# Performance work log

Measured on AMD Instinct MI355X. Metric: run time of the kernel, lower is better.

## Reference

```python
import jax, jax.numpy as jnp
from jax import lax
import numpy as np


def _rnn_tanh_layer(x, W_ih, W_hh, b_ih, b_hh, return_seq):
    # x: [B, T, I]; W_ih: [H, I]; W_hh: [H, H]
    B = x.shape[0]
    H = W_hh.shape[0]
    # Precompute input projection for all timesteps (one big GEMM).
    xw = jnp.einsum('bti,hi->bth', x, W_ih) + b_ih + b_hh  # [B, T, H]
    xw_t = jnp.swapaxes(xw, 0, 1)  # [T, B, H] for scan
    h0 = jnp.zeros((B, H), dtype=x.dtype)

    def step(h, xt):
        h_new = jnp.tanh(xt + h @ W_hh.T)
        return h_new, (h_new if return_seq else None)

    hT, hs = lax.scan(step, h0, xw_t)
    if return_seq:
        return jnp.swapaxes(hs, 0, 1), hT  # [B, T, H], [B, H]
    return None, hT


def setup_inputs() -> dict:
    key = jax.random.key(0)
    ks = jax.random.split(key, 12)
    B, T, I, H1, H2, C = 512, 1024, 32, 128, 64, 10

    def unif(k, shape, fan):
        bound = 1.0 / np.sqrt(fan)
        return jax.random.uniform(k, shape, jnp.float32, -bound, bound)

    return {
        'x': jax.random.normal(ks[0], (B, T, I), jnp.float32),
        'W_ih1': unif(ks[1], (H1, I), H1),
        'W_hh1': unif(ks[2], (H1, H1), H1),
        'b_ih1': unif(ks[3], (H1,), H1),
        'b_hh1': unif(ks[4], (H1,), H1),
        'W_ih2': unif(ks[5], (H2, H1), H2),
        'W_hh2': unif(ks[6], (H2, H2), H2),
        'b_ih2': unif(ks[7], (H2,), H2),
        'b_hh2': unif(ks[8], (H2,), H2),
        'W_fc': unif(ks[9], (C, H2), H2),
        'b_fc': unif(ks[10], (C,), H2),
    }


def reference(x, W_ih1, W_hh1, b_ih1, b_hh1, W_ih2, W_hh2, b_ih2, b_hh2, W_fc, b_fc):
    out1, _h1 = _rnn_tanh_layer(x, W_ih1, W_hh1, b_ih1, b_hh1, return_seq=True)
    _none, h2 = _rnn_tanh_layer(out1, W_ih2, W_hh2, b_ih2, b_hh2, return_seq=False)
    # Dropout(p=0.3) is identity in eval mode.
    logits = h2 @ W_fc.T + b_fc  # [B, 10]
    return logits
```

## Files before the change

kernel.cpp:

```cpp
#include <hip/hip_runtime.h>
#include <stdint.h>


typedef _Float16 f16x8 __attribute__((ext_vector_type(8)));
typedef _Float16 f16x4 __attribute__((ext_vector_type(4)));
typedef float f32x4 __attribute__((ext_vector_type(4)));

#define MFMA_F16(A, B, C) __builtin_amdgcn_mfma_f32_16x16x32_f16((A), (B), (C), 0, 0, 0)

__device__ __forceinline__ float tanh_fast(float x) {
  float t = __builtin_amdgcn_exp2f(x * 2.88539008177792681472f);
  return 1.0f - 2.0f * __builtin_amdgcn_rcpf(t + 1.0f);
}

__device__ __forceinline__ uint32_t pk16(float a, float b) {
  return __builtin_bit_cast(uint32_t, __builtin_amdgcn_cvt_pkrtz(a, b));
}

__device__ __forceinline__ void sync_lds() {
  asm volatile("s_waitcnt lgkmcnt(0)\n\ts_barrier" ::: "memory");
}

__device__ __forceinline__ f16x8 cvt8w(const float* s) {
  f32x4 a = *(const f32x4*)s;
  f32x4 b = *(const f32x4*)(s + 4);
  f16x8 r;
#pragma unroll
  for (int j = 0; j < 4; ++j) { r[j] = (_Float16)a[j]; r[4 + j] = (_Float16)b[j]; }
  return r;
}

__device__ __forceinline__ f16x8 pack_x8(const f32x4& a, const f32x4& b) {
  union { uint32_t u[4]; f16x8 v; } tmp;
  tmp.u[0] = pk16(a[0], a[1]); tmp.u[1] = pk16(a[2], a[3]);
  tmp.u[2] = pk16(b[0], b[1]); tmp.u[3] = pk16(b[2], b[3]);
  return tmp.v;
}

__global__ __launch_bounds__(256) void xw_pre(
    const float* __restrict__ x, const float* __restrict__ Wih1,
    const float* __restrict__ bih1, const float* __restrict__ bhh1,
    uint2* __restrict__ xw)
{
  const int tid  = threadIdx.x;
  const int w    = tid >> 6, lane = tid & 63;
  const int g    = lane >> 4, n = lane & 15;
  const int gb   = blockIdx.x >> 3;
  const int t0   = ((blockIdx.x & 7) << 7) + (w << 5);

  f16x8 aI[8];
  f32x4 bias[8];
#pragma unroll
  for (int m = 0; m < 8; ++m) {
    aI[m] = cvt8w(Wih1 + (m * 16 + n) * 32 + g * 8);
#pragma unroll
    for (int r = 0; r < 4; ++r)
      bias[m][r] = bih1[m * 16 + g * 4 + r] + bhh1[m * 16 + g * 4 + r];
  }

  const float* xp = x + ((size_t)(gb * 16 + n) * 1024 + t0) * 32 + g * 8;
  uint2* xo = xw + (size_t)(gb * 1024 + t0) * 512 + lane;

  f32x4 xa = *(const f32x4*)(xp);
  f32x4 xb = *(const f32x4*)(xp + 4);
  for (int tt = 0; tt < 32; ++tt) {
    f32x4 na, nb;
    if (tt < 31) {
      na = *(const f32x4*)(xp + (tt + 1) * 32);
      nb = *(const f32x4*)(xp + (tt + 1) * 32 + 4);
    }
    f16x8 xf = pack_x8(xa, xb);
#pragma unroll
    for (int m = 0; m < 8; ++m) {
      f32x4 d = MFMA_F16(aI[m], xf, bias[m]);
      xo[tt * 512 + m * 64] = make_uint2(pk16(d[0], d[1]), pk16(d[2], d[3]));
    }
    xa = na; xb = nb;
  }
}

template <bool USE_XW>
__global__ __attribute__((amdgpu_waves_per_eu(2, 2))) __launch_bounds__(512)
void rnn_rec(
    const float* __restrict__ x,
    const float* __restrict__ Wih1, const float* __restrict__ Whh1,
    const float* __restrict__ bih1, const float* __restrict__ bhh1,
    const float* __restrict__ Wih2, const float* __restrict__ Whh2,
    const float* __restrict__ bih2, const float* __restrict__ bhh2,
    const float* __restrict__ Wfc,  const float* __restrict__ bfc,
    const uint2* __restrict__ xw,
    float* __restrict__ out)
{
  constexpr int T = 1024, I = 32, H1 = 128, H2 = 64, BB = 16;
  constexpr int R1 = 272, R2 = 144;
  constexpr int H1_0 = 0, H1_1 = 4352;
  constexpr int H2_0 = 8704, H2_1 = 11008;
  constexpr int H2F  = 13312;
  __shared__ __align__(16) unsigned char smem[17408];

  const int tid  = threadIdx.x;
  const int w    = tid >> 6;
  const int lane = tid & 63;
  const int g    = lane >> 4;
  const int n    = lane & 15;
  const int b0   = blockIdx.x * BB;

  {
    uint32_t* p = (uint32_t*)smem;
    for (int i = tid; i < 1088; i += 512) p[i] = 0u;
    uint32_t* q = (uint32_t*)(smem + H2_0);
    for (int i = tid; i < 576; i += 512) q[i] = 0u;
  }

  int roff1[4];
#pragma unroll
  for (int k4 = 0; k4 < 4; ++k4)
    roff1[k4] = n * R1 + k4 * 64 + g * 16;

  auto tanh_pack = [&](const f32x4& a, uint32_t& lo, uint32_t& hi) {
    lo = pk16(tanh_fast(a[0]), tanh_fast(a[1]));
    hi = pk16(tanh_fast(a[2]), tanh_fast(a[3]));
  };

  __syncthreads();

  const f32x4 zero = {0.f, 0.f, 0.f, 0.f};

  if (w < 4) {
    f16x8 aU[2][4];
#pragma unroll
    for (int ti = 0; ti < 2; ++ti) {
      const int ch = (2 * w + ti) * 16 + n;
#pragma unroll
      for (int k4 = 0; k4 < 4; ++k4)
        aU[ti][k4] = cvt8w(Whh1 + ch * H1 + k4 * 32 + g * 8);
    }
    int woff[2];
#pragma unroll
    for (int ti = 0; ti < 2; ++ti)
      woff[ti] = n * R1 + (2 * w + ti) * 32 + g * 8;

    if constexpr (USE_XW) {
      const uint2* xwp = xw + (size_t)blockIdx.x * T * 512 + lane;
      const int ti0 = (2 * w) * 64, ti1 = (2 * w + 1) * 64;

      auto cvtC = [](uint2 v) -> f32x4 {
        f16x4 h = __builtin_bit_cast(f16x4, v);
        f32x4 r;
#pragma unroll
        for (int i = 0; i < 4; ++i) r[i] = (float)h[i];
        return r;
      };

      uint2 qA0 = xwp[0 * 512 + ti0], qA1 = xwp[0 * 512 + ti1];
      uint2 qB0 = xwp[1 * 512 + ti0], qB1 = xwp[1 * 512 + ti1];

      auto stepL1 = [&](int t, int cur, uint2& s0, uint2& s1) {
        const char* H1c = (const char*)smem + (cur ? H1_1 : H1_0);
        char*       H1n = (char*)smem + (cur ? H1_0 : H1_1);
        f16x8 b1k0 = *(const f16x8*)(H1c + roff1[0]);
        f16x8 b1k1 = *(const f16x8*)(H1c + roff1[1]);
        f16x8 b1k2 = *(const f16x8*)(H1c + roff1[2]);
        f16x8 b1k3 = *(const f16x8*)(H1c + roff1[3]);
        f32x4 accI0 = cvtC(s0), accI1 = cvtC(s1);
        if (t + 2 < T) {
          s0 = xwp[(t + 2) * 512 + ti0];
          s1 = xwp[(t + 2) * 512 + ti1];
        }
        f32x4 aA0 = MFMA_F16(aU[0][0], b1k0, accI0);
        f32x4 aB0 = MFMA_F16(aU[0][2], b1k2, zero);
        f32x4 aA1 = MFMA_F16(aU[1][0], b1k0, accI1);
        f32x4 aB1 = MFMA_F16(aU[1][2], b1k2, zero);
        aA0 = MFMA_F16(aU[0][1], b1k1, aA0);
        aB0 = MFMA_F16(aU[0][3], b1k3, aB0);
        aA1 = MFMA_F16(aU[1][1], b1k1, aA1);
        aB1 = MFMA_F16(aU[1][3], b1k3, aB1);
        {
          f32x4 s0v = aA0 + aB0;
          uint32_t lo, hi;
          tanh_pack(s0v, lo, hi);
          *(uint2*)(H1n + woff[0]) = make_uint2(lo, hi);
        }
        {
          f32x4 s1v = aA1 + aB1;
          uint32_t lo, hi;
          tanh_pack(s1v, lo, hi);
          *(uint2*)(H1n + woff[1]) = make_uint2(lo, hi);
        }
        sync_lds();
      };

      for (int t = 0; t < T; t += 2) {
        stepL1(t + 0, 0, qA0, qA1);
        stepL1(t + 1, 1, qB0, qB1);
      }
    } else {
      f16x8 aI1[2];
      f32x4 bias1[2];
#pragma unroll
      for (int ti = 0; ti < 2; ++ti) {
        const int ch = (2 * w + ti) * 16 + n;
        aI1[ti] = cvt8w(Wih1 + ch * I + g * 8);
        const int cb = (2 * w + ti) * 16 + g * 4;
#pragma unroll
        for (int r = 0; r < 4; ++r) bias1[ti][r] = bih1[cb + r] + bhh1[cb + r];
      }
      const float* xp = x + (size_t)(b0 + n) * T * I + g * 8;
      f32x4 q0a = *(const f32x4*)(xp + 0 * I), q0b = *(const f32x4*)(xp + 0 * I + 4);
      f32x4 q1a = *(const f32x4*)(xp + 1 * I), q1b = *(const f32x4*)(xp + 1 * I + 4);
      f32x4 q2a = *(const f32x4*)(xp + 2 * I), q2b = *(const f32x4*)(xp + 2 * I + 4);
      f32x4 q3a = *(const f32x4*)(xp + 3 * I), q3b = *(const f32x4*)(xp + 3 * I + 4);

      f32x4 accI0, accI1;
      {
        f16x8 xf = pack_x8(q0a, q0b);
        accI0 = MFMA_F16(aI1[0], xf, bias1[0]);
        accI1 = MFMA_F16(aI1[1], xf, bias1[1]);
      }

      auto stepL1 = [&](int t, int cur, f32x4& la, f32x4& lb,
                        const f32x4& pa, const f32x4& pb) {
        const char* H1c = (const char*)smem + (cur ? H1_1 : H1_0);
        char*       H1n = (char*)smem + (cur ? H1_0 : H1_1);
        f16x8 b1k0 = *(const f16x8*)(H1c + roff1[0]);
        f16x8 b1k1 = *(const f16x8*)(H1c + roff1[1]);
        f16x8 b1k2 = *(const f16x8*)(H1c + roff1[2]);
        f16x8 b1k3 = *(const f16x8*)(H1c + roff1[3]);
        if (t + 4 < T) {
          la = *(const f32x4*)(xp + (t + 4) * I);
          lb = *(const f32x4*)(xp + (t + 4) * I + 4);
        }
        f32x4 aA0 = MFMA_F16(aU[0][0], b1k0, accI0);
        f32x4 aB0 = MFMA_F16(aU[0][2], b1k2, zero);
        f32x4 aA1 = MFMA_F16(aU[1][0], b1k0, accI1);
        f32x4 aB1 = MFMA_F16(aU[1][2], b1k2, zero);
        aA0 = MFMA_F16(aU[0][1], b1k1, aA0);
        aB0 = MFMA_F16(aU[0][3], b1k3, aB0);
        aA1 = MFMA_F16(aU[1][1], b1k1, aA1);
        aB1 = MFMA_F16(aU[1][3], b1k3, aB1);
        {
          f16x8 xf = pack_x8(pa, pb);
          accI0 = MFMA_F16(aI1[0], xf, bias1[0]);
          accI1 = MFMA_F16(aI1[1], xf, bias1[1]);
        }
        {
          f32x4 s0 = aA0 + aB0;
          uint32_t lo, hi;
          tanh_pack(s0, lo, hi);
          *(uint2*)(H1n + woff[0]) = make_uint2(lo, hi);
        }
        {
          f32x4 s1 = aA1 + aB1;
          uint32_t lo, hi;
          tanh_pack(s1, lo, hi);
          *(uint2*)(H1n + woff[1]) = make_uint2(lo, hi);
        }
        sync_lds();
      };

      for (int t = 0; t < T; t += 4) {
        stepL1(t + 0, 0, q0a, q0b, q1a, q1b);
        stepL1(t + 1, 1, q1a, q1b, q2a, q2b);
        stepL1(t + 2, 0, q2a, q2b, q3a, q3b);
        stepL1(t + 3, 1, q3a, q3b, q0a, q0b);
      }
    }
  } else {
    const int j = w - 4;
    f16x8 aI2[4], aR2[2];
#pragma unroll
    for (int k4 = 0; k4 < 4; ++k4)
      aI2[k4] = cvt8w(Wih2 + (16 * j + n) * H1 + k4 * 32 + g * 8);
#pragma unroll
    for (int k2 = 0; k2 < 2; ++k2)
      aR2[k2] = cvt8w(Whh2 + (16 * j + n) * H2 + k2 * 32 + g * 8);
    f32x4 bias2;
#pragma unroll
    for (int r = 0; r < 4; ++r) bias2[r] = bih2[16 * j + g * 4 + r] + bhh2[16 * j + g * 4 + r];

    int roff2[2];
#pragma unroll
    for (int k2 = 0; k2 < 2; ++k2)
      roff2[k2] = n * R2 + k2 * 64 + g * 16;
    const int woff2 = n * R2 + j * 32 + g * 8;

    auto l2_body = [&](const char* H1c, const char* H2r, f32x4& s) {
      f16x8 b1k0 = *(const f16x8*)(H1c + roff1[0]);
      f16x8 b1k1 = *(const f16x8*)(H1c + roff1[1]);
      f16x8 b1k2 = *(const f16x8*)(H1c + roff1[2]);
      f16x8 b1k3 = *(const f16x8*)(H1c + roff1[3]);
      f16x8 b2k0 = *(const f16x8*)(H2r + roff2[0]);
      f16x8 b2k1 = *(const f16x8*)(H2r + roff2[1]);
      f32x4 cA = MFMA_F16(aI2[0], b1k0, bias2);
      f32x4 cB = MFMA_F16(aI2[1], b1k1, zero);
      f32x4 cC = MFMA_F16(aR2[0], b2k0, zero);
      cA = MFMA_F16(aI2[2], b1k2, cA);
      cB = MFMA_F16(aI2[3], b1k3, cB);
      cC = MFMA_F16(aR2[1], b2k1, cC);
      s = cA + cB + cC;
    };

    auto stepL2 = [&](int t, int cur) {
      if (t > 0) {
        const char* H1c = (const char*)smem + (cur ? H1_1 : H1_0);
        const char* H2r = (const char*)smem + (cur ? H2_0 : H2_1);
        char*       H2w = (char*)smem + (cur ? H2_1 : H2_0);
        f32x4 s;
        l2_body(H1c, H2r, s);
        uint32_t lo, hi;
        tanh_pack(s, lo, hi);
        *(uint2*)(H2w + woff2) = make_uint2(lo, hi);
      }
      sync_lds();
    };

    for (int t = 0; t < T; t += 2) {
      stepL2(t + 0, 0);
      stepL2(t + 1, 1);
    }

    {
      f32x4 s;
      l2_body((const char*)smem + H1_0, (const char*)smem + H2_1, s);
      f32x4 hv;
#pragma unroll
      for (int r = 0; r < 4; ++r) hv[r] = tanh_fast(s[r]);
      *(f32x4*)(smem + H2F + n * 256 + (16 * j + 4 * g) * 4) = hv;
    }
  }

  sync_lds();

  if (tid < BB * 10) {
    const int b = tid / 10, c = tid % 10;
    const float* hrow = (const float*)(smem + H2F + b * 256);
    float acc = bfc[c];
#pragma unroll 8
    for (int k = 0; k < 64; ++k) acc += hrow[k] * Wfc[c * 64 + k];
    out[(size_t)(b0 + b) * 10 + c] = acc;
  }
}

extern "C" void kernel_launch(void* const* d_in, const int* in_sizes, int n_in,
                              void* d_out, int out_size, void* d_ws, size_t ws_size,
                              hipStream_t stream) {
  const float* x    = (const float*)d_in[0];
  const float* Wih1 = (const float*)d_in[1];
  const float* Whh1 = (const float*)d_in[2];
  const float* bih1 = (const float*)d_in[3];
  const float* bhh1 = (const float*)d_in[4];
  const float* Wih2 = (const float*)d_in[5];
  const float* Whh2 = (const float*)d_in[6];
  const float* bih2 = (const float*)d_in[7];
  const float* bhh2 = (const float*)d_in[8];
  const float* Wfc  = (const float*)d_in[9];
  const float* bfc  = (const float*)d_in[10];

  const size_t xw_bytes = (size_t)512 * 1024 * 128 * 2;
  if (ws_size >= xw_bytes) {
    uint2* xw = (uint2*)d_ws;
    hipLaunchKernelGGL(xw_pre, dim3(256), dim3(256), 0, stream,
                       x, Wih1, bih1, bhh1, xw);
    hipLaunchKernelGGL((rnn_rec<true>), dim3(512 / 16), dim3(512), 0, stream,
                       x, Wih1, Whh1, bih1, bhh1, Wih2, Whh2, bih2, bhh2,
                       Wfc, bfc, (const uint2*)xw, (float*)d_out);
  } else {
    hipLaunchKernelGGL((rnn_rec<false>), dim3(512 / 16), dim3(512), 0, stream,
                       x, Wih1, Whh1, bih1, bhh1, Wih2, Whh2, bih2, bhh2,
                       Wfc, bfc, (const uint2*)nullptr, (float*)d_out);
  }
}
```

Before: 433.1 us.

## Move layer-2 input projection into layer-1 waves and shorten layer-2 critical path

Layer-1 waves now also compute the layer-2 input projection (Wih2 · h1_t) right after reading h1 and write it as fp32 partials to a double-buffered LDS region. Layer-2 waves then only apply the small Whh2 recurrence on top of the partial, so layer 2 lags one extra step. This cuts the MFMA chain per step on the layer-2 side and balances work across the barrier-synchronized waves. The LDS layout also changes to an unpadded fragment-major form so each lane reads its 16 bytes contiguously, and LDS usage grows. The old no-workspace path is kept as a separate simplified fallback kernel.

```diff
diff --git a/kernel.cpp b/kernel.cpp
--- a/kernel.cpp
+++ b/kernel.cpp
@@ -79,16 +79,223 @@
   }
 }
 
-template <bool USE_XW>
 __global__ __attribute__((amdgpu_waves_per_eu(2, 2))) __launch_bounds__(512)
 void rnn_rec(
+    const float* __restrict__ Whh1,
+    const float* __restrict__ Wih2, const float* __restrict__ Whh2,
+    const float* __restrict__ bih2, const float* __restrict__ bhh2,
+    const float* __restrict__ Wfc,  const float* __restrict__ bfc,
+    const uint2* __restrict__ xw,
+    float* __restrict__ out)
+{
+  constexpr int T = 1024, H1 = 128, H2 = 64, BB = 16;
+  constexpr int H1_0 = 0,     H1_1 = 4096;
+  constexpr int H2_0 = 8192,  H2_1 = 10240;
+  constexpr int PB_0 = 12288, PB_1 = 16384;
+  constexpr int H2F  = 20480;
+  __shared__ __align__(16) unsigned char smem[24576];
+
+  const int tid  = threadIdx.x;
+  const int w    = tid >> 6;
+  const int lane = tid & 63;
+  const int g    = lane >> 4;
+  const int n    = lane & 15;
+  const int b0   = blockIdx.x * BB;
+
+  {
+    uint32_t* p = (uint32_t*)smem;
+    for (int i = tid; i < 1024; i += 512) p[i] = 0u;
+    uint32_t* q = (uint32_t*)(smem + H2_0);
+    for (int i = tid; i < 1024; i += 512) q[i] = 0u;
+  }
+
+  auto tanh_pack = [&](const f32x4& a, uint32_t& lo, uint32_t& hi) {
+    lo = pk16(tanh_fast(a[0]), tanh_fast(a[1]));
+    hi = pk16(tanh_fast(a[2]), tanh_fast(a[3]));
+  };
+
+  __syncthreads();
+
+  const f32x4 zero = {0.f, 0.f, 0.f, 0.f};
+  const int lb = lane * 16;
+
+  if (w < 4) {
+    f16x8 aU[2][4], aI2[4];
+    f32x4 bias2v;
+#pragma unroll
+    for (int ti = 0; ti < 2; ++ti) {
+      const int ch = (2 * w + ti) * 16 + n;
+#pragma unroll
+      for (int k4 = 0; k4 < 4; ++k4)
+        aU[ti][k4] = cvt8w(Whh1 + ch * H1 + k4 * 32 + g * 8);
+    }
+#pragma unroll
+    for (int k4 = 0; k4 < 4; ++k4)
+      aI2[k4] = cvt8w(Wih2 + (16 * w + n) * H1 + k4 * 32 + g * 8);
+#pragma unroll
+    for (int r = 0; r < 4; ++r)
+      bias2v[r] = bih2[16 * w + g * 4 + r] + bhh2[16 * w + g * 4 + r];
+
+    int woff[2];
+#pragma unroll
+    for (int ti = 0; ti < 2; ++ti)
+      woff[ti] = w * 1024 + (2 * ti + (g >> 1)) * 256 + n * 16 + (g & 1) * 8;
+    const int pw_rel = w * 1024 + lb;
+
+    const uint2* xwp = xw + (size_t)blockIdx.x * T * 512 + lane;
+    const int ti0 = (2 * w) * 64, ti1 = (2 * w + 1) * 64;
+
+    auto cvtC = [](uint2 v) -> f32x4 {
+      f16x4 h = __builtin_bit_cast(f16x4, v);
+      f32x4 r;
+#pragma unroll
+      for (int i = 0; i < 4; ++i) r[i] = (float)h[i];
+      return r;
+    };
+
+    uint2 qA0 = xwp[0 * 512 + ti0], qA1 = xwp[0 * 512 + ti1];
+    uint2 qB0 = xwp[1 * 512 + ti0], qB1 = xwp[1 * 512 + ti1];
+
+    auto stepL1 = [&](int t, int cur, uint2& s0, uint2& s1) {
+      const char* H1c = (const char*)smem + (cur ? H1_1 : H1_0);
+      char*       H1n = (char*)smem + (cur ? H1_0 : H1_1);
+      char*       Pw  = (char*)smem + (cur ? PB_1 : PB_0);
+      f16x8 b1k0 = *(const f16x8*)(H1c + 0 * 1024 + lb);
+      f16x8 b1k1 = *(const f16x8*)(H1c + 1 * 1024 + lb);
+      f16x8 b1k2 = *(const f16x8*)(H1c + 2 * 1024 + lb);
+      f16x8 b1k3 = *(const f16x8*)(H1c + 3 * 1024 + lb);
+      f32x4 accI0 = cvtC(s0), accI1 = cvtC(s1);
+      if (t + 2 < T) {
+        s0 = xwp[(t + 2) * 512 + ti0];
+        s1 = xwp[(t + 2) * 512 + ti1];
+      }
+      f32x4 aA0 = MFMA_F16(aU[0][0], b1k0, accI0);
+      f32x4 aB0 = MFMA_F16(aU[0][2], b1k2, zero);
+      f32x4 aA1 = MFMA_F16(aU[1][0], b1k0, accI1);
+      f32x4 aB1 = MFMA_F16(aU[1][2], b1k2, zero);
+      aA0 = MFMA_F16(aU[0][1], b1k1, aA0);
+      aB0 = MFMA_F16(aU[0][3], b1k3, aB0);
+      aA1 = MFMA_F16(aU[1][1], b1k1, aA1);
+      aB1 = MFMA_F16(aU[1][3], b1k3, aB1);
+      {
+        f32x4 cA = MFMA_F16(aI2[0], b1k0, bias2v);
+        f32x4 cB = MFMA_F16(aI2[1], b1k1, zero);
+        cA = MFMA_F16(aI2[2], b1k2, cA);
+        cB = MFMA_F16(aI2[3], b1k3, cB);
+        *(f32x4*)(Pw + pw_rel) = cA + cB;
+      }
+      {
+        f32x4 s0v = aA0 + aB0;
+        uint32_t lo, hi;
+        tanh_pack(s0v, lo, hi);
+        *(uint2*)(H1n + woff[0]) = make_uint2(lo, hi);
+      }
+      {
+        f32x4 s1v = aA1 + aB1;
+        uint32_t lo, hi;
+        tanh_pack(s1v, lo, hi);
+        *(uint2*)(H1n + woff[1]) = make_uint2(lo, hi);
+      }
+      sync_lds();
+    };
+
+    for (int t = 0; t < T; t += 2) {
+      stepL1(t + 0, 0, qA0, qA1);
+      stepL1(t + 1, 1, qB0, qB1);
+    }
+    {
+      const char* H1c = (const char*)smem + H1_0;
+      f16x8 b1k0 = *(const f16x8*)(H1c + 0 * 1024 + lb);
+      f16x8 b1k1 = *(const f16x8*)(H1c + 1 * 1024 + lb);
+      f16x8 b1k2 = *(const f16x8*)(H1c + 2 * 1024 + lb);
+      f16x8 b1k3 = *(const f16x8*)(H1c + 3 * 1024 + lb);
+      f32x4 cA = MFMA_F16(aI2[0], b1k0, bias2v);
+      f32x4 cB = MFMA_F16(aI2[1], b1k1, zero);
+      cA = MFMA_F16(aI2[2], b1k2, cA);
+      cB = MFMA_F16(aI2[3], b1k3, cB);
+      *(f32x4*)((char*)smem + PB_0 + pw_rel) = cA + cB;
+    }
+    sync_lds();
+    sync_lds();
+  } else {
+    const int j2 = w - 4;
+    f16x8 aR2[2];
+#pragma unroll
+    for (int k2 = 0; k2 < 2; ++k2)
+      aR2[k2] = cvt8w(Whh2 + (16 * j2 + n) * H2 + k2 * 32 + g * 8);
+
+    const int h2w = (j2 >> 1) * 1024 + (2 * (j2 & 1) + (g >> 1)) * 256
+                  + n * 16 + (g & 1) * 8;
+    const int proff = j2 * 1024 + lb;
+
+    auto stepL2 = [&](int s, int cur) {
+      if (s > 1) {
+        const char* Pr  = (const char*)smem + (cur ? PB_0 : PB_1);
+        const char* H2r = (const char*)smem + (cur ? H2_1 : H2_0);
+        char*       H2w = (char*)smem + (cur ? H2_0 : H2_1);
+        f32x4 part = *(const f32x4*)(Pr + proff);
+        f16x8 b2k0 = *(const f16x8*)(H2r + 0 * 1024 + lb);
+        f16x8 b2k1 = *(const f16x8*)(H2r + 1 * 1024 + lb);
+        f32x4 z2 = MFMA_F16(aR2[0], b2k0, part);
+        z2 = MFMA_F16(aR2[1], b2k1, z2);
+        uint32_t lo, hi;
+        tanh_pack(z2, lo, hi);
+        *(uint2*)(H2w + h2w) = make_uint2(lo, hi);
+      }
+      sync_lds();
+    };
+
+    for (int s = 0; s < T; s += 2) {
+      stepL2(s + 0, 0);
+      stepL2(s + 1, 1);
+    }
+    {
+      const char* Pr  = (const char*)smem + PB_1;
+      const char* H2r = (const char*)smem + H2_0;
+      char*       H2w = (char*)smem + H2_1;
+      f32x4 part = *(const f32x4*)(Pr + proff);
+      f16x8 b2k0 = *(const f16x8*)(H2r + 0 * 1024 + lb);
+      f16x8 b2k1 = *(const f16x8*)(H2r + 1 * 1024 + lb);
+      f32x4 z2 = MFMA_F16(aR2[0], b2k0, part);
+      z2 = MFMA_F16(aR2[1], b2k1, z2);
+      uint32_t lo, hi;
+      tanh_pack(z2, lo, hi);
+      *(uint2*)(H2w + h2w) = make_uint2(lo, hi);
+    }
+    sync_lds();
+    {
+      const char* Pr  = (const char*)smem + PB_0;
+      const char* H2r = (const char*)smem + H2_1;
+      f32x4 part = *(const f32x4*)(Pr + proff);
+      f16x8 b2k0 = *(const f16x8*)(H2r + 0 * 1024 + lb);
+      f16x8 b2k1 = *(const f16x8*)(H2r + 1 * 1024 + lb);
+      f32x4 z2 = MFMA_F16(aR2[0], b2k0, part);
+      z2 = MFMA_F16(aR2[1], b2k1, z2);
+      f32x4 hv;
+#pragma unroll
+      for (int r = 0; r < 4; ++r) hv[r] = tanh_fast(z2[r]);
+      *(f32x4*)(smem + H2F + n * 256 + (16 * j2 + 4 * g) * 4) = hv;
+    }
+    sync_lds();
+  }
+
+  if (tid < BB * 10) {
+    const int b = tid / 10, c = tid % 10;
+    const float* hrow = (const float*)(smem + H2F + b * 256);
+    float acc = bfc[c];
+#pragma unroll 8
+    for (int k = 0; k < 64; ++k) acc += hrow[k] * Wfc[c * 64 + k];
+    out[(size_t)(b0 + b) * 10 + c] = acc;
+  }
+}
+
+__global__ __launch_bounds__(512) void rnn_fallback(
     const float* __restrict__ x,
     const float* __restrict__ Wih1, const float* __restrict__ Whh1,
     const float* __restrict__ bih1, const float* __restrict__ bhh1,
     const float* __restrict__ Wih2, const float* __restrict__ Whh2,
     const float* __restrict__ bih2, const float* __restrict__ bhh2,
     const float* __restrict__ Wfc,  const float* __restrict__ bfc,
-    const uint2* __restrict__ xw,
     float* __restrict__ out)
 {
   constexpr int T = 1024, I = 32, H1 = 128, H2 = 64, BB = 16;
@@ -97,173 +304,82 @@
   constexpr int H2_0 = 8704, H2_1 = 11008;
   constexpr int H2F  = 13312;
   __shared__ __align__(16) unsigned char smem[17408];
-
-  const int tid  = threadIdx.x;
-  const int w    = tid >> 6;
-  const int lane = tid & 63;
-  const int g    = lane >> 4;
-  const int n    = lane & 15;
-  const int b0   = blockIdx.x * BB;
-
+  const int tid = threadIdx.x, w = tid >> 6, lane = tid & 63;
+  const int g = lane >> 4, n = lane & 15, b0 = blockIdx.x * BB;
   {
     uint32_t* p = (uint32_t*)smem;
     for (int i = tid; i < 1088; i += 512) p[i] = 0u;
     uint32_t* q = (uint32_t*)(smem + H2_0);
     for (int i = tid; i < 576; i += 512) q[i] = 0u;
   }
-
   int roff1[4];
 #pragma unroll
-  for (int k4 = 0; k4 < 4; ++k4)
-    roff1[k4] = n * R1 + k4 * 64 + g * 16;
-
+  for (int k4 = 0; k4 < 4; ++k4) roff1[k4] = n * R1 + k4 * 64 + g * 16;
   auto tanh_pack = [&](const f32x4& a, uint32_t& lo, uint32_t& hi) {
     lo = pk16(tanh_fast(a[0]), tanh_fast(a[1]));
     hi = pk16(tanh_fast(a[2]), tanh_fast(a[3]));
   };
-
   __syncthreads();
-
   const f32x4 zero = {0.f, 0.f, 0.f, 0.f};
-
   if (w < 4) {
-    f16x8 aU[2][4];
+    f16x8 aU[2][4], aI1[2];
+    f32x4 bias1[2];
 #pragma unroll
     for (int ti = 0; ti < 2; ++ti) {
       const int ch = (2 * w + ti) * 16 + n;
 #pragma unroll
       for (int k4 = 0; k4 < 4; ++k4)
         aU[ti][k4] = cvt8w(Whh1 + ch * H1 + k4 * 32 + g * 8);
+      aI1[ti] = cvt8w(Wih1 + ch * I + g * 8);
+      const int cb = (2 * w + ti) * 16 + g * 4;
+#pragma unroll
+      for (int r = 0; r < 4; ++r) bias1[ti][r] = bih1[cb + r] + bhh1[cb + r];
     }
     int woff[2];
 #pragma unroll
     for (int ti = 0; ti < 2; ++ti)
       woff[ti] = n * R1 + (2 * w + ti) * 32 + g * 8;
-
-    if constexpr (USE_XW) {
-      const uint2* xwp = xw + (size_t)blockIdx.x * T * 512 + lane;
-      const int ti0 = (2 * w) * 64, ti1 = (2 * w + 1) * 64;
-
-      auto cvtC = [](uint2 v) -> f32x4 {
-        f16x4 h = __builtin_bit_cast(f16x4, v);
-        f32x4 r;
-#pragma unroll
-        for (int i = 0; i < 4; ++i) r[i] = (float)h[i];
-        return r;
-      };
-
-      uint2 qA0 = xwp[0 * 512 + ti0], qA1 = xwp[0 * 512 + ti1];
-      uint2 qB0 = xwp[1 * 512 + ti0], qB1 = xwp[1 * 512 + ti1];
-
-      auto stepL1 = [&](int t, int cur, uint2& s0, uint2& s1) {
-        const char* H1c = (const char*)smem + (cur ? H1_1 : H1_0);
-        char*       H1n = (char*)smem + (cur ? H1_0 : H1_1);
-        f16x8 b1k0 = *(const f16x8*)(H1c + roff1[0]);
-        f16x8 b1k1 = *(const f16x8*)(H1c + roff1[1]);
-        f16x8 b1k2 = *(const f16x8*)(H1c + roff1[2]);
-        f16x8 b1k3 = *(const f16x8*)(H1c + roff1[3]);
-        f32x4 accI0 = cvtC(s0), accI1 = cvtC(s1);
-        if (t + 2 < T) {
-          s0 = xwp[(t + 2) * 512 + ti0];
-          s1 = xwp[(t + 2) * 512 + ti1];
-        }
-        f32x4 aA0 = MFMA_F16(aU[0][0], b1k0, accI0);
-        f32x4 aB0 = MFMA_F16(aU[0][2], b1k2, zero);
-        f32x4 aA1 = MFMA_F16(aU[1][0], b1k0, accI1);
-        f32x4 aB1 = MFMA_F16(aU[1][2], b1k2, zero);
-        aA0 = MFMA_F16(aU[0][1], b1k1, aA0);
-        aB0 = MFMA_F16(aU[0][3], b1k3, aB0);
-        aA1 = MFMA_F16(aU[1][1], b1k1, aA1);
-        aB1 = MFMA_F16(aU[1][3], b1k3, aB1);
-        {
-          f32x4 s0v = aA0 + aB0;
-          uint32_t lo, hi;
-          tanh_pack(s0v, lo, hi);
-          *(uint2*)(H1n + woff[0]) = make_uint2(lo, hi);
-        }
-        {
-          f32x4 s1v = aA1 + aB1;
-          uint32_t lo, hi;
-          tanh_pack(s1v, lo, hi);
-          *(uint2*)(H1n + woff[1]) = make_uint2(lo, hi);
-        }
-        sync_lds();
-      };
-
-      for (int t = 0; t < T; t += 2) {
-        stepL1(t + 0, 0, qA0, qA1);
-        stepL1(t + 1, 1, qB0, qB1);
-      }
-    } else {
-      f16x8 aI1[2];
-      f32x4 bias1[2];
-#pragma unroll
-      for (int ti = 0; ti < 2; ++ti) {
-        const int ch = (2 * w + ti) * 16 + n;
-        aI1[ti] = cvt8w(Wih1 + ch * I + g * 8);
-        const int cb = (2 * w + ti) * 16 + g * 4;
-#pragma unroll
-        for (int r = 0; r < 4; ++r) bias1[ti][r] = bih1[cb + r] + bhh1[cb + r];
-      }
-      const float* xp = x + (size_t)(b0 + n) * T * I + g * 8;
-      f32x4 q0a = *(const f32x4*)(xp + 0 * I), q0b = *(const f32x4*)(xp + 0 * I + 4);
-      f32x4 q1a = *(const f32x4*)(xp + 1 * I), q1b = *(const f32x4*)(xp + 1 * I + 4);
-      f32x4 q2a = *(const f32x4*)(xp + 2 * I), q2b = *(const f32x4*)(xp + 2 * I + 4);
-      f32x4 q3a = *(const f32x4*)(xp + 3 * I), q3b = *(const f32x4*)(xp + 3 * I + 4);
-
-      f32x4 accI0, accI1;
-      {
-        f16x8 xf = pack_x8(q0a, q0b);
+    const float* xp = x + (size_t)(b0 + n) * T * I + g * 8;
+    f32x4 qa = *(const f32x4*)(xp), qb = *(const f32x4*)(xp + 4);
+    f32x4 accI0, accI1;
+    {
+      f16x8 xf = pack_x8(qa, qb);
+      accI0 = MFMA_F16(aI1[0], xf, bias1[0]);
+      accI1 = MFMA_F16(aI1[1], xf, bias1[1]);
+    }
+    for (int t = 0; t < T; ++t) {
+      const int cur = t & 1;
+      const char* H1c = (const char*)smem + (cur ? H1_1 : H1_0);
+      char*       H1n = (char*)smem + (cur ? H1_0 : H1_1);
+      f16x8 b1k0 = *(const f16x8*)(H1c + roff1[0]);
+      f16x8 b1k1 = *(const f16x8*)(H1c + roff1[1]);
+      f16x8 b1k2 = *(const f16x8*)(H1c + roff1[2]);
+      f16x8 b1k3 = *(const f16x8*)(H1c + roff1[3]);
+      if (t + 1 < T) {
+        qa = *(const f32x4*)(xp + (t + 1) * I);
+        qb = *(const f32x4*)(xp + (t + 1) * I + 4);
+      }
+      f32x4 aA0 = MFMA_F16(aU[0][0], b1k0, accI0);
+      f32x4 aB0 = MFMA_F16(aU[0][2], b1k2, zero);
+      f32x4 aA1 = MFMA_F16(aU[1][0], b1k0, accI1);
+      f32x4 aB1 = MFMA_F16(aU[1][2], b1k2, zero);
+      aA0 = MFMA_F16(aU[0][1], b1k1, aA0);
+      aB0 = MFMA_F16(aU[0][3], b1k3, aB0);
+      aA1 = MFMA_F16(aU[1][1], b1k1, aA1);
+      aB1 = MFMA_F16(aU[1][3], b1k3, aB1);
+      if (t + 1 < T) {
+        f16x8 xf = pack_x8(qa, qb);
         accI0 = MFMA_F16(aI1[0], xf, bias1[0]);
         accI1 = MFMA_F16(aI1[1], xf, bias1[1]);
       }
-
-      auto stepL1 = [&](int t, int cur, f32x4& la, f32x4& lb,
-                        const f32x4& pa, const f32x4& pb) {
-        const char* H1c = (const char*)smem + (cur ? H1_1 : H1_0);
-        char*       H1n = (char*)smem + (cur ? H1_0 : H1_1);
-        f16x8 b1k0 = *(const f16x8*)(H1c + roff1[0]);
-        f16x8 b1k1 = *(const f16x8*)(H1c + roff1[1]);
-        f16x8 b1k2 = *(const f16x8*)(H1c + roff1[2]);
-        f16x8 b1k3 = *(const f16x8*)(H1c + roff1[3]);
-        if (t + 4 < T) {
-          la = *(const f32x4*)(xp + (t + 4) * I);
-          lb = *(const f32x4*)(xp + (t + 4) * I + 4);
-        }
-        f32x4 aA0 = MFMA_F16(aU[0][0], b1k0, accI0);
-        f32x4 aB0 = MFMA_F16(aU[0][2], b1k2, zero);
-        f32x4 aA1 = MFMA_F16(aU[1][0], b1k0, accI1);
-        f32x4 aB1 = MFMA_F16(aU[1][2], b1k2, zero);
-        aA0 = MFMA_F16(aU[0][1], b1k1, aA0);
-        aB0 = MFMA_F16(aU[0][3], b1k3, aB0);
-        aA1 = MFMA_F16(aU[1][1], b1k1, aA1);
-        aB1 = MFMA_F16(aU[1][3], b1k3, aB1);
-        {
-          f16x8 xf = pack_x8(pa, pb);
-          accI0 = MFMA_F16(aI1[0], xf, bias1[0]);
-          accI1 = MFMA_F16(aI1[1], xf, bias1[1]);
-        }
-        {
-          f32x4 s0 = aA0 + aB0;
-          uint32_t lo, hi;
-          tanh_pack(s0, lo, hi);
-          *(uint2*)(H1n + woff[0]) = make_uint2(lo, hi);
-        }
-        {
-          f32x4 s1 = aA1 + aB1;
-          uint32_t lo, hi;
-          tanh_pack(s1, lo, hi);
-          *(uint2*)(H1n + woff[1]) = make_uint2(lo, hi);
-        }
-        sync_lds();
-      };
-
-      for (int t = 0; t < T; t += 4) {
-        stepL1(t + 0, 0, q0a, q0b, q1a, q1b);
-        stepL1(t + 1, 1, q1a, q1b, q2a, q2b);
-        stepL1(t + 2, 0, q2a, q2b, q3a, q3b);
-        stepL1(t + 3, 1, q3a, q3b, q0a, q0b);
-      }
+      uint32_t lo, hi;
+      f32x4 s0 = aA0 + aB0;
+      tanh_pack(s0, lo, hi);
+      *(uint2*)(H1n + woff[0]) = make_uint2(lo, hi);
+      f32x4 s1 = aA1 + aB1;
+      tanh_pack(s1, lo, hi);
+      *(uint2*)(H1n + woff[1]) = make_uint2(lo, hi);
+      sync_lds();
     }
   } else {
     const int j = w - 4;
@@ -276,14 +392,12 @@
       aR2[k2] = cvt8w(Whh2 + (16 * j + n) * H2 + k2 * 32 + g * 8);
     f32x4 bias2;
 #pragma unroll
-    for (int r = 0; r < 4; ++r) bias2[r] = bih2[16 * j + g * 4 + r] + bhh2[16 * j + g * 4 + r];
-
+    for (int r = 0; r < 4; ++r)
+      bias2[r] = bih2[16 * j + g * 4 + r] + bhh2[16 * j + g * 4 + r];
     int roff2[2];
 #pragma unroll
-    for (int k2 = 0; k2 < 2; ++k2)
-      roff2[k2] = n * R2 + k2 * 64 + g * 16;
+    for (int k2 = 0; k2 < 2; ++k2) roff2[k2] = n * R2 + k2 * 64 + g * 16;
     const int woff2 = n * R2 + j * 32 + g * 8;
-
     auto l2_body = [&](const char* H1c, const char* H2r, f32x4& s) {
       f16x8 b1k0 = *(const f16x8*)(H1c + roff1[0]);
       f16x8 b1k1 = *(const f16x8*)(H1c + roff1[1]);
@@ -299,8 +413,8 @@
       cC = MFMA_F16(aR2[1], b2k1, cC);
       s = cA + cB + cC;
     };
-
-    auto stepL2 = [&](int t, int cur) {
+    for (int t = 0; t < T; ++t) {
+      const int cur = t & 1;
       if (t > 0) {
         const char* H1c = (const char*)smem + (cur ? H1_1 : H1_0);
         const char* H2r = (const char*)smem + (cur ? H2_0 : H2_1);
@@ -312,13 +426,7 @@
         *(uint2*)(H2w + woff2) = make_uint2(lo, hi);
       }
       sync_lds();
-    };
-
-    for (int t = 0; t < T; t += 2) {
-      stepL2(t + 0, 0);
-      stepL2(t + 1, 1);
-    }
-
+    }
     {
       f32x4 s;
       l2_body((const char*)smem + H1_0, (const char*)smem + H2_1, s);
@@ -328,9 +436,7 @@
       *(f32x4*)(smem + H2F + n * 256 + (16 * j + 4 * g) * 4) = hv;
     }
   }
-
   sync_lds();
-
   if (tid < BB * 10) {
     const int b = tid / 10, c = tid % 10;
     const float* hrow = (const float*)(smem + H2F + b * 256);
@@ -361,12 +467,12 @@
     uint2* xw = (uint2*)d_ws;
     hipLaunchKernelGGL(xw_pre, dim3(256), dim3(256), 0, stream,
                        x, Wih1, bih1, bhh1, xw);
-    hipLaunchKernelGGL((rnn_rec<true>), dim3(512 / 16), dim3(512), 0, stream,
+    hipLaunchKernelGGL(rnn_rec, dim3(512 / 16), dim3(512), 0, stream,
+                       Whh1, Wih2, Whh2, bih2, bhh2, Wfc, bfc,
+                       (const uint2*)xw, (float*)d_out);
+  } else {
+    hipLaunchKernelGGL(rnn_fallback, dim3(512 / 16), dim3(512), 0, stream,
                        x, Wih1, Whh1, bih1, bhh1, Wih2, Whh2, bih2, bhh2,
-                       Wfc, bfc, (const uint2*)xw, (float*)d_out);
-  } else {
-    hipLaunchKernelGGL((rnn_rec<false>), dim3(512 / 16), dim3(512), 0, stream,
-                       x, Wih1, Whh1, bih1, bhh1, Wih2, Whh2, bih2, bhh2,
-                       Wfc, bfc, (const uint2*)nullptr, (float*)d_out);
-  }
-}
+                       Wfc, bfc, (float*)d_out);
+  }
+}
```

New measurement: 495.7 us. 1.14x slower.
